# Kernel tuning notes

Measured on AMD Instinct MI355X. Metric: run time of the kernel, lower is better.

## Reference

```python
import jax, jax.numpy as jnp
import numpy as np
import math

B, N, C, H, CH = 1, 256, 128, 4, 32  # batch, n_res, pair channels, heads, head dim
LN_EPS = 1e-5


def setup_inputs() -> dict:
    key = jax.random.key(0)
    ks = jax.random.split(key, 12)
    s = 0.02
    return {
        "act": jax.random.normal(ks[0], (B, N, N, C), dtype=jnp.float32),
        "mask": (jax.random.uniform(ks[1], (B, N, N)) < 0.9).astype(jnp.float32),
        "ln_g": jnp.ones((C,), jnp.float32),
        "ln_b": jnp.zeros((C,), jnp.float32),
        "wq": jax.random.normal(ks[2], (C, H * CH), jnp.float32) * s,
        "wk": jax.random.normal(ks[3], (C, H * CH), jnp.float32) * s,
        "wv": jax.random.normal(ks[4], (C, H * CH), jnp.float32) * s,
        "w2d": jax.random.normal(ks[5], (C, H), jnp.float32) * s,
        "wg": jax.random.normal(ks[6], (C, H * CH), jnp.float32) * s,
        "bg": jnp.ones((H * CH,), jnp.float32),
        "wo": jax.random.normal(ks[7], (H * CH, C), jnp.float32) * s,
        "bo": jnp.zeros((C,), jnp.float32),
    }


def reference(act, mask, ln_g, ln_b, wq, wk, wv, w2d, wg, bg, wo, bo):
    # swap the two residue axes: attend along the *starting* node axis
    x = jnp.swapaxes(act, -2, -3)          # [b, m, i, C]
    m = jnp.swapaxes(mask, -1, -2)         # [b, m, i]
    # LayerNorm
    mu = jnp.mean(x, axis=-1, keepdims=True)
    var = jnp.var(x, axis=-1, keepdims=True)
    x = (x - mu) * jax.lax.rsqrt(var + LN_EPS) * ln_g + ln_b
    # additive mask bias: [b, m, 1, 1, i]
    bias = (1e9 * (m - 1.0))[..., :, None, None, :]
    shp = x.shape[:-1]
    q = (x @ wq).reshape(*shp, H, CH)
    k = (x @ wk).reshape(*shp, H, CH)
    v = (x @ wv).reshape(*shp, H, CH)
    factor = 1.0 / math.sqrt(CH)
    aff = jnp.einsum('bmihc,bmjhc->bmhij', q * factor, k) + bias
    # non-batched pair bias: [b, h, m, i]; broadcasts against [b, m, h, i, j]
    # exactly as in the torch code (requires b == 1)
    nb = jnp.transpose(x @ w2d, (0, 3, 1, 2))
    weights = jax.nn.softmax(aff + nb, axis=-1)  # [b, m, h, i, j]
    g = jax.nn.sigmoid((x @ wg + bg).reshape(*shp, H, CH))
    out = jnp.einsum('bmhqk,bmkhc->bmqhc', weights, v) * g
    out = out.reshape(*shp, H * CH) @ wo + bo
    return jnp.swapaxes(out, -2, -3)
```

## Files before the change

kernel.cpp:

```cpp
#include <hip/hip_runtime.h>
#include <hip/hip_bf16.h>
#include <math.h>


typedef __attribute__((ext_vector_type(8))) short short8;
typedef __attribute__((ext_vector_type(4))) short short4v;
typedef __attribute__((ext_vector_type(4))) float f32x4;

__device__ __forceinline__ unsigned short f2bf(float f) {
  __hip_bfloat16 b = __float2bfloat16(f);
  return __builtin_bit_cast(unsigned short, b);
}
__device__ __forceinline__ float bf2f(unsigned short u) {
  return __uint_as_float(((unsigned int)u) << 16);
}

__device__ __forceinline__ f32x4 mfma16(short8 a, short8 b, f32x4 c) {
  return __builtin_amdgcn_mfma_f32_16x16x32_bf16(a, b, c, 0, 0, 0);
}

__global__ __launch_bounds__(256) void k_conv(const float* __restrict__ wq,
                                              const float* __restrict__ wk,
                                              const float* __restrict__ wv,
                                              const float* __restrict__ wg,
                                              const float* __restrict__ w2d,
                                              const float* __restrict__ wo,
                                              const float* __restrict__ mask,
                                              unsigned short* __restrict__ Wt4,
                                              unsigned short* __restrict__ Wto,
                                              float* __restrict__ maskT) {
  int idx = blockIdx.x * 256 + threadIdx.x;
  if (idx < 65536) {
    int n = idx >> 7, k = idx & 127;
    const float* ws = (n < 128) ? wq : (n < 256) ? wk : (n < 384) ? wv : wg;
    Wt4[idx] = f2bf(ws[k * 128 + (n & 127)]);
  } else if (idx < 73728) {
    int j = idx - 65536;
    int r = j >> 7, k = j & 127;
    Wt4[idx] = (r < 4) ? f2bf(w2d[k * 4 + r]) : (unsigned short)0;
  } else if (idx < 90112) {
    int j = idx - 73728;
    int n = j >> 7, k = j & 127;
    Wto[j] = f2bf(wo[k * 128 + n]);
  } else if (idx < 155648) {
    int j2 = idx - 90112;
    int mi = j2 & 255, jj = j2 >> 8;
    maskT[mi * 256 + jj] = 1e9f * (mask[jj * 256 + mi] - 1.0f);
  }
}

__global__ __launch_bounds__(256) void k_ln(const float* __restrict__ act,
                                            const float* __restrict__ ln_g,
                                            const float* __restrict__ ln_b,
                                            unsigned short* __restrict__ lnxb) {
  int t = threadIdx.x;
  int grp = t >> 4, l16 = t & 15;
  int row = blockIdx.x * 16 + grp;
  int mm = row >> 8, ii = row & 255;
  const float4* a = (const float4*)(act + ((size_t)(ii * 256 + mm)) * 128);
  float4 v0 = a[l16 * 2], v1 = a[l16 * 2 + 1];
  float s = (v0.x + v0.y) + (v0.z + v0.w) + (v1.x + v1.y) + (v1.z + v1.w);
  #pragma unroll
  for (int off = 1; off < 16; off <<= 1) s += __shfl_xor(s, off, 64);
  float mean = s * (1.f / 128.f);
  float e[8] = {v0.x - mean, v0.y - mean, v0.z - mean, v0.w - mean,
                v1.x - mean, v1.y - mean, v1.z - mean, v1.w - mean};
  float vs = (e[0]*e[0] + e[1]*e[1]) + (e[2]*e[2] + e[3]*e[3]) +
             (e[4]*e[4] + e[5]*e[5]) + (e[6]*e[6] + e[7]*e[7]);
  #pragma unroll
  for (int off = 1; off < 16; off <<= 1) vs += __shfl_xor(vs, off, 64);
  float rstd = rsqrtf(vs * (1.f / 128.f) + 1e-5f);
  const float4* gp = (const float4*)ln_g;
  const float4* bp = (const float4*)ln_b;
  float4 g0 = gp[l16 * 2], g1 = gp[l16 * 2 + 1];
  float4 b0 = bp[l16 * 2], b1 = bp[l16 * 2 + 1];
  short8 o;
  o[0] = (short)f2bf(e[0] * rstd * g0.x + b0.x);
  o[1] = (short)f2bf(e[1] * rstd * g0.y + b0.y);
  o[2] = (short)f2bf(e[2] * rstd * g0.z + b0.z);
  o[3] = (short)f2bf(e[3] * rstd * g0.w + b0.w);
  o[4] = (short)f2bf(e[4] * rstd * g1.x + b1.x);
  o[5] = (short)f2bf(e[5] * rstd * g1.y + b1.y);
  o[6] = (short)f2bf(e[6] * rstd * g1.z + b1.z);
  o[7] = (short)f2bf(e[7] * rstd * g1.w + b1.w);
  *(short8*)(lnxb + (size_t)row * 128 + l16 * 8) = o;
}

__global__ __launch_bounds__(256) void k_projg(const unsigned short* __restrict__ A,
                                               const unsigned short* __restrict__ Bt,
                                               const float* __restrict__ bg,
                                               unsigned short* __restrict__ qb,
                                               unsigned short* __restrict__ kb,
                                               unsigned short* __restrict__ vb,
                                               unsigned short* __restrict__ sgb,
                                               float* __restrict__ b2t) {
  __shared__ unsigned short As[128 * 40];
  __shared__ unsigned short Bs[64 * 40];
  int t = threadIdx.x;
  int m0 = blockIdx.x * 128, n0 = blockIdx.y * 64;
  int w = t >> 6, l = t & 63, g = l >> 4, li = l & 15;
  int wr = w >> 1, wc = w & 1;
  f32x4 acc[4][2] = {};
  for (int s = 0; s < 4; ++s) {
    int k0 = s * 32;
    __syncthreads();
    {
      int row = t >> 1, kl = (t & 1) * 16;
      const short8* src = (const short8*)(A + (size_t)(m0 + row) * 128 + k0 + kl);
      *(short8*)&As[row * 40 + kl]     = src[0];
      *(short8*)&As[row * 40 + kl + 8] = src[1];
      int bn = t >> 2, bk = (t & 3) * 8;
      *(short8*)&Bs[bn * 40 + bk] = *(const short8*)(Bt + (size_t)(n0 + bn) * 128 + k0 + bk);
    }
    __syncthreads();
    short8 af[4], bf[2];
    #pragma unroll
    for (int it = 0; it < 4; ++it)
      af[it] = *(const short8*)&As[(wr * 64 + it * 16 + li) * 40 + g * 8];
    #pragma unroll
    for (int jt = 0; jt < 2; ++jt)
      bf[jt] = *(const short8*)&Bs[(wc * 32 + jt * 16 + li) * 40 + g * 8];
    #pragma unroll
    for (int it = 0; it < 4; ++it)
      #pragma unroll
      for (int jt = 0; jt < 2; ++jt)
        acc[it][jt] = mfma16(af[it], bf[jt], acc[it][jt]);
  }
  int which = n0 >> 7;
  if (which == 4) {
    #pragma unroll
    for (int it = 0; it < 4; ++it)
      #pragma unroll
      for (int jt = 0; jt < 2; ++jt) {
        int hb = (wc * 32 + jt * 16 + li);
        if (hb < 4) {
          #pragma unroll
          for (int r = 0; r < 4; ++r) {
            int R = m0 + wr * 64 + it * 16 + g * 4 + r;
            b2t[(size_t)hb * 65536 + (R & 255) * 256 + (R >> 8)] = acc[it][jt][r];
          }
        }
      }
    return;
  }
  const float factor = 0.17677669529663687f;
  #pragma unroll
  for (int it = 0; it < 4; ++it)
    #pragma unroll
    for (int jt = 0; jt < 2; ++jt) {
      int n = n0 + wc * 32 + jt * 16 + li;
      int hh = (n >> 5) & 3, ch = n & 31;
      #pragma unroll
      for (int r = 0; r < 4; ++r) {
        int R = m0 + wr * 64 + it * 16 + g * 4 + r;
        int mm = R >> 8, ii = R & 255;
        size_t o = ((size_t)((mm * 4 + hh) * 256 + ii)) * 32 + ch;
        float v = acc[it][jt][r];
        if (which == 0)      qb[o] = f2bf(v * factor);
        else if (which == 1) kb[o] = f2bf(v);
        else if (which == 2) vb[o] = f2bf(v);
        else                 sgb[o] = f2bf(1.f / (1.f + __expf(-(v + bg[n & 127]))));
      }
    }
}

__global__ __launch_bounds__(256) void k_attn(const unsigned short* __restrict__ qb,
                                              const unsigned short* __restrict__ kb,
                                              const unsigned short* __restrict__ vb,
                                              const unsigned short* __restrict__ sgb,
                                              const float* __restrict__ b2t,
                                              const float* __restrict__ maskT,
                                              unsigned short* __restrict__ aob) {
  __shared__ unsigned short VT[32 * 264];
  __shared__ unsigned short Pl[4 * 32 * 72];
  __shared__ float maskls[256];
  int m = blockIdx.x >> 1, ihalf = blockIdx.x & 1, h = blockIdx.y;
  int t = threadIdx.x, w = t >> 6, l = t & 63, g = l >> 4, li = l & 15;
  int base = (m * 4 + h) << 8;
  maskls[t] = maskT[m * 256 + t];
  {
    const unsigned int* v32 = (const unsigned int*)(vb + (size_t)base * 32);
    #pragma unroll
    for (int p = 0; p < 16; ++p) {
      int idx = t + p * 256;
      int j = idx >> 4, cp = idx & 15;
      unsigned int u = v32[idx];
      VT[(cp * 2) * 264 + j]     = (unsigned short)(u & 0xffff);
      VT[(cp * 2 + 1) * 264 + j] = (unsigned short)(u >> 16);
    }
  }
  __syncthreads();
  int i0 = ihalf * 128 + w * 32;
  short8 qf[2];
  #pragma unroll
  for (int it = 0; it < 2; ++it)
    qf[it] = *(const short8*)(qb + ((size_t)(base + i0 + it * 16 + li)) * 32 + g * 8);
  float mst[2] = {-1e30f, -1e30f};
  float lst[2] = {0.f, 0.f};
  f32x4 oacc[2][2] = {};
  const float* b2 = b2t + (size_t)h * 65536;
  unsigned short* Pw = Pl + w * 32 * 72;
  for (int jc = 0; jc < 4; ++jc) {
    int j0 = jc * 64;
    f32x4 sacc[4][2];
    #pragma unroll
    for (int jt = 0; jt < 4; ++jt) {
      short8 kf = *(const short8*)(kb + ((size_t)(base + j0 + jt * 16 + li)) * 32 + g * 8);
      #pragma unroll
      for (int it = 0; it < 2; ++it) {
        f32x4 z = {0.f, 0.f, 0.f, 0.f};
        sacc[jt][it] = mfma16(kf, qf[it], z);
      }
    }
    #pragma unroll
    for (int it = 0; it < 2; ++it) {
      int ic = i0 + it * 16 + li;
      float s[16];
      float cmax = -1e30f;
      #pragma unroll
      for (int jt = 0; jt < 4; ++jt) {
        int jb = j0 + jt * 16 + g * 4;
        f32x4 mk = *(const f32x4*)&maskls[jb];
        #pragma unroll
        for (int r = 0; r < 4; ++r) {
          float sv = sacc[jt][it][r] + b2[(size_t)(jb + r) * 256 + ic] + mk[r];
          s[jt * 4 + r] = sv;
          cmax = fmaxf(cmax, sv);
        }
      }
      cmax = fmaxf(cmax, __shfl_xor(cmax, 16));
      cmax = fmaxf(cmax, __shfl_xor(cmax, 32));
      float mnew = fmaxf(mst[it], cmax);
      float fac = __expf(mst[it] - mnew);
      mst[it] = mnew;
      lst[it] *= fac;
      oacc[0][it] *= fac;
      oacc[1][it] *= fac;
      float psum = 0.f;
      #pragma unroll
      for (int jt = 0; jt < 4; ++jt) {
        float p0 = __expf(s[jt * 4 + 0] - mnew);
        float p1 = __expf(s[jt * 4 + 1] - mnew);
        float p2 = __expf(s[jt * 4 + 2] - mnew);
        float p3 = __expf(s[jt * 4 + 3] - mnew);
        psum += p0 + p1 + p2 + p3;
        short4v pk;
        pk.x = (short)f2bf(p0); pk.y = (short)f2bf(p1);
        pk.z = (short)f2bf(p2); pk.w = (short)f2bf(p3);
        *(short4v*)&Pw[(it * 16 + li) * 72 + jt * 16 + g * 4] = pk;
      }
      lst[it] += psum;
    }
    asm volatile("" ::: "memory");
    #pragma unroll
    for (int ks = 0; ks < 2; ++ks) {
      short8 vf0 = *(const short8*)&VT[li * 264        + j0 + ks * 32 + g * 8];
      short8 vf1 = *(const short8*)&VT[(16 + li) * 264 + j0 + ks * 32 + g * 8];
      #pragma unroll
      for (int it = 0; it < 2; ++it) {
        short8 pf = *(const short8*)&Pw[(it * 16 + li) * 72 + ks * 32 + g * 8];
        oacc[0][it] = mfma16(vf0, pf, oacc[0][it]);
        oacc[1][it] = mfma16(vf1, pf, oacc[1][it]);
      }
    }
    asm volatile("" ::: "memory");
  }
  #pragma unroll
  for (int it = 0; it < 2; ++it) {
    float lt = lst[it];
    lt += __shfl_xor(lt, 16);
    lt += __shfl_xor(lt, 32);
    float inv = 1.f / lt;
    int ic = i0 + it * 16 + li;
    #pragma unroll
    for (int ct = 0; ct < 2; ++ct) {
      int c0 = ct * 16 + g * 4;
      const unsigned short* grow = sgb + ((size_t)(base + ic)) * 32 + c0;
      ushort4 gu = *(const ushort4*)grow;
      ushort4 ov;
      ov.x = f2bf(oacc[ct][it][0] * inv * bf2f(gu.x));
      ov.y = f2bf(oacc[ct][it][1] * inv * bf2f(gu.y));
      ov.z = f2bf(oacc[ct][it][2] * inv * bf2f(gu.z));
      ov.w = f2bf(oacc[ct][it][3] * inv * bf2f(gu.w));
      *(ushort4*)&aob[((size_t)(ic * 256 + m)) * 128 + h * 32 + c0] = ov;
    }
  }
}

__global__ __launch_bounds__(256) void k_outg(const unsigned short* __restrict__ A,
                                              const unsigned short* __restrict__ Bt,
                                              const float* __restrict__ bo,
                                              float* __restrict__ out) {
  __shared__ unsigned short As[128 * 40];
  __shared__ unsigned short Bs[64 * 40];
  int t = threadIdx.x;
  int m0 = blockIdx.x * 128, n0 = blockIdx.y * 64;
  int w = t >> 6, l = t & 63, g = l >> 4, li = l & 15;
  int wr = w >> 1, wc = w & 1;
  f32x4 acc[4][2] = {};
  for (int s = 0; s < 4; ++s) {
    int k0 = s * 32;
    __syncthreads();
    {
      int row = t >> 1, kl = (t & 1) * 16;
      const short8* src = (const short8*)(A + (size_t)(m0 + row) * 128 + k0 + kl);
      *(short8*)&As[row * 40 + kl]     = src[0];
      *(short8*)&As[row * 40 + kl + 8] = src[1];
      int bn = t >> 2, bk = (t & 3) * 8;
      *(short8*)&Bs[bn * 40 + bk] = *(const short8*)(Bt + (size_t)(n0 + bn) * 128 + k0 + bk);
    }
    __syncthreads();
    short8 af[4], bf[2];
    #pragma unroll
    for (int it = 0; it < 4; ++it)
      af[it] = *(const short8*)&As[(wr * 64 + it * 16 + li) * 40 + g * 8];
    #pragma unroll
    for (int jt = 0; jt < 2; ++jt)
      bf[jt] = *(const short8*)&Bs[(wc * 32 + jt * 16 + li) * 40 + g * 8];
    #pragma unroll
    for (int it = 0; it < 4; ++it)
      #pragma unroll
      for (int jt = 0; jt < 2; ++jt)
        acc[it][jt] = mfma16(af[it], bf[jt], acc[it][jt]);
  }
  #pragma unroll
  for (int it = 0; it < 4; ++it)
    #pragma unroll
    for (int jt = 0; jt < 2; ++jt) {
      int n = n0 + wc * 32 + jt * 16 + li;
      float bias = bo[n];
      #pragma unroll
      for (int r = 0; r < 4; ++r) {
        int R = m0 + wr * 64 + it * 16 + g * 4 + r;
        out[(size_t)R * 128 + n] = acc[it][jt][r] + bias;
      }
    }
}

extern "C" void kernel_launch(void* const* d_in, const int* in_sizes, int n_in,
                              void* d_out, int out_size, void* d_ws, size_t ws_size,
                              hipStream_t stream) {
  const float* act  = (const float*)d_in[0];
  const float* mask = (const float*)d_in[1];
  const float* ln_g = (const float*)d_in[2];
  const float* ln_b = (const float*)d_in[3];
  const float* wq   = (const float*)d_in[4];
  const float* wk   = (const float*)d_in[5];
  const float* wv   = (const float*)d_in[6];
  const float* w2d  = (const float*)d_in[7];
  const float* wg   = (const float*)d_in[8];
  const float* bg   = (const float*)d_in[9];
  const float* wo   = (const float*)d_in[10];
  const float* bo   = (const float*)d_in[11];

  char* p = (char*)d_ws;
  unsigned short* lnxb  = (unsigned short*)p;  p += (size_t)8388608 * 2;
  float*          b2t   = (float*)p;           p += (size_t)262144 * 4;
  unsigned short* qb    = (unsigned short*)p;  p += (size_t)8388608 * 2;
  unsigned short* kb    = (unsigned short*)p;  p += (size_t)8388608 * 2;
  unsigned short* vb    = (unsigned short*)p;  p += (size_t)8388608 * 2;
  unsigned short* sgb   = (unsigned short*)p;  p += (size_t)8388608 * 2;
  unsigned short* aob   = (unsigned short*)p;  p += (size_t)8388608 * 2;
  unsigned short* Wt4   = (unsigned short*)p;  p += (size_t)73728 * 2;
  unsigned short* Wto   = (unsigned short*)p;  p += (size_t)16384 * 2;
  float*          maskT = (float*)p;           p += (size_t)65536 * 4;
  float* out = (float*)d_out;

  hipLaunchKernelGGL(k_conv,  dim3(608),      dim3(256), 0, stream, wq, wk, wv, wg, w2d, wo, mask, Wt4, Wto, maskT);
  hipLaunchKernelGGL(k_ln,    dim3(4096),     dim3(256), 0, stream, act, ln_g, ln_b, lnxb);
  hipLaunchKernelGGL(k_projg, dim3(512, 9),   dim3(256), 0, stream, lnxb, Wt4, bg, qb, kb, vb, sgb, b2t);
  hipLaunchKernelGGL(k_attn,  dim3(512, 4),   dim3(256), 0, stream, qb, kb, vb, sgb, b2t, maskT, aob);
  hipLaunchKernelGGL(k_outg,  dim3(512, 2),   dim3(256), 0, stream, aob, Wto, bo, out);
}
```

Measured before the change: 104.0 us.

## Merge weight conversion into LayerNorm launch and vectorize GEMM epilogue stores

Folds the weight/mask conversion kernel into the LayerNorm kernel as extra blocks, which removes one launch. It also swaps the MFMA operand order so each lane holds four consecutive output columns. The projection and output epilogues can then write packed 4-wide bf16 or float4 stores instead of scalar strided stores. The pair-bias path is rewritten to match the transposed accumulator layout.

```diff
diff --git a/kernel.cpp b/kernel.cpp
--- a/kernel.cpp
+++ b/kernel.cpp
@@ -19,41 +19,42 @@
   return __builtin_amdgcn_mfma_f32_16x16x32_bf16(a, b, c, 0, 0, 0);
 }
 
-__global__ __launch_bounds__(256) void k_conv(const float* __restrict__ wq,
-                                              const float* __restrict__ wk,
-                                              const float* __restrict__ wv,
-                                              const float* __restrict__ wg,
-                                              const float* __restrict__ w2d,
-                                              const float* __restrict__ wo,
-                                              const float* __restrict__ mask,
-                                              unsigned short* __restrict__ Wt4,
-                                              unsigned short* __restrict__ Wto,
-                                              float* __restrict__ maskT) {
-  int idx = blockIdx.x * 256 + threadIdx.x;
-  if (idx < 65536) {
-    int n = idx >> 7, k = idx & 127;
-    const float* ws = (n < 128) ? wq : (n < 256) ? wk : (n < 384) ? wv : wg;
-    Wt4[idx] = f2bf(ws[k * 128 + (n & 127)]);
-  } else if (idx < 73728) {
-    int j = idx - 65536;
-    int r = j >> 7, k = j & 127;
-    Wt4[idx] = (r < 4) ? f2bf(w2d[k * 4 + r]) : (unsigned short)0;
-  } else if (idx < 90112) {
-    int j = idx - 73728;
-    int n = j >> 7, k = j & 127;
-    Wto[j] = f2bf(wo[k * 128 + n]);
-  } else if (idx < 155648) {
-    int j2 = idx - 90112;
-    int mi = j2 & 255, jj = j2 >> 8;
-    maskT[mi * 256 + jj] = 1e9f * (mask[jj * 256 + mi] - 1.0f);
-  }
-}
-
 __global__ __launch_bounds__(256) void k_ln(const float* __restrict__ act,
                                             const float* __restrict__ ln_g,
                                             const float* __restrict__ ln_b,
-                                            unsigned short* __restrict__ lnxb) {
+                                            const float* __restrict__ wq,
+                                            const float* __restrict__ wk,
+                                            const float* __restrict__ wv,
+                                            const float* __restrict__ wg,
+                                            const float* __restrict__ w2d,
+                                            const float* __restrict__ wo,
+                                            const float* __restrict__ mask,
+                                            unsigned short* __restrict__ lnxb,
+                                            unsigned short* __restrict__ Wt4,
+                                            unsigned short* __restrict__ Wto,
+                                            float* __restrict__ maskT) {
   int t = threadIdx.x;
+  if (blockIdx.x >= 4096) {
+    int idx = (blockIdx.x - 4096) * 256 + t;
+    if (idx < 65536) {
+      int n = idx >> 7, k = idx & 127;
+      const float* ws = (n < 128) ? wq : (n < 256) ? wk : (n < 384) ? wv : wg;
+      Wt4[idx] = f2bf(ws[k * 128 + (n & 127)]);
+    } else if (idx < 73728) {
+      int j = idx - 65536;
+      int r = j >> 7, k = j & 127;
+      Wt4[idx] = (r < 4) ? f2bf(w2d[k * 4 + r]) : (unsigned short)0;
+    } else if (idx < 90112) {
+      int j = idx - 73728;
+      int n = j >> 7, k = j & 127;
+      Wto[j] = f2bf(wo[k * 128 + n]);
+    } else if (idx < 155648) {
+      int j2 = idx - 90112;
+      int mi = j2 & 255, jj = j2 >> 8;
+      maskT[mi * 256 + jj] = 1e9f * (mask[jj * 256 + mi] - 1.0f);
+    }
+    return;
+  }
   int grp = t >> 4, l16 = t & 15;
   int row = blockIdx.x * 16 + grp;
   int mm = row >> 8, ii = row & 255;
@@ -124,44 +125,53 @@
     for (int it = 0; it < 4; ++it)
       #pragma unroll
       for (int jt = 0; jt < 2; ++jt)
-        acc[it][jt] = mfma16(af[it], bf[jt], acc[it][jt]);
+        acc[it][jt] = mfma16(bf[jt], af[it], acc[it][jt]);
   }
   int which = n0 >> 7;
   if (which == 4) {
-    #pragma unroll
-    for (int it = 0; it < 4; ++it)
-      #pragma unroll
-      for (int jt = 0; jt < 2; ++jt) {
-        int hb = (wc * 32 + jt * 16 + li);
-        if (hb < 4) {
-          #pragma unroll
-          for (int r = 0; r < 4; ++r) {
-            int R = m0 + wr * 64 + it * 16 + g * 4 + r;
-            b2t[(size_t)hb * 65536 + (R & 255) * 256 + (R >> 8)] = acc[it][jt][r];
-          }
-        }
-      }
+    if (wc == 0 && g == 0) {
+      #pragma unroll
+      for (int it = 0; it < 4; ++it) {
+        int R = m0 + wr * 64 + it * 16 + li;
+        int mm = R >> 8, ii = R & 255;
+        #pragma unroll
+        for (int r = 0; r < 4; ++r)
+          b2t[(size_t)r * 65536 + ii * 256 + mm] = acc[it][0][r];
+      }
+    }
     return;
   }
   const float factor = 0.17677669529663687f;
   #pragma unroll
-  for (int it = 0; it < 4; ++it)
+  for (int it = 0; it < 4; ++it) {
+    int R = m0 + wr * 64 + it * 16 + li;
+    int mm = R >> 8, ii = R & 255;
     #pragma unroll
     for (int jt = 0; jt < 2; ++jt) {
-      int n = n0 + wc * 32 + jt * 16 + li;
-      int hh = (n >> 5) & 3, ch = n & 31;
-      #pragma unroll
-      for (int r = 0; r < 4; ++r) {
-        int R = m0 + wr * 64 + it * 16 + g * 4 + r;
-        int mm = R >> 8, ii = R & 255;
-        size_t o = ((size_t)((mm * 4 + hh) * 256 + ii)) * 32 + ch;
-        float v = acc[it][jt][r];
-        if (which == 0)      qb[o] = f2bf(v * factor);
-        else if (which == 1) kb[o] = f2bf(v);
-        else if (which == 2) vb[o] = f2bf(v);
-        else                 sgb[o] = f2bf(1.f / (1.f + __expf(-(v + bg[n & 127]))));
-      }
-    }
+      int nb4 = n0 + wc * 32 + jt * 16 + g * 4;
+      int hh = (nb4 >> 5) & 3, ch = nb4 & 31;
+      size_t o = ((size_t)((mm * 4 + hh) * 256 + ii)) * 32 + ch;
+      short4v pk;
+      if (which == 0) {
+        #pragma unroll
+        for (int r = 0; r < 4; ++r) pk[r] = (short)f2bf(acc[it][jt][r] * factor);
+        *(short4v*)(qb + o) = pk;
+      } else if (which == 1) {
+        #pragma unroll
+        for (int r = 0; r < 4; ++r) pk[r] = (short)f2bf(acc[it][jt][r]);
+        *(short4v*)(kb + o) = pk;
+      } else if (which == 2) {
+        #pragma unroll
+        for (int r = 0; r < 4; ++r) pk[r] = (short)f2bf(acc[it][jt][r]);
+        *(short4v*)(vb + o) = pk;
+      } else {
+        #pragma unroll
+        for (int r = 0; r < 4; ++r)
+          pk[r] = (short)f2bf(1.f / (1.f + __expf(-(acc[it][jt][r] + bg[(nb4 & 127) + r]))));
+        *(short4v*)(sgb + o) = pk;
+      }
+    }
+  }
 }
 
 __global__ __launch_bounds__(256) void k_attn(const unsigned short* __restrict__ qb,
@@ -321,20 +331,22 @@
     for (int it = 0; it < 4; ++it)
       #pragma unroll
       for (int jt = 0; jt < 2; ++jt)
-        acc[it][jt] = mfma16(af[it], bf[jt], acc[it][jt]);
-  }
-  #pragma unroll
-  for (int it = 0; it < 4; ++it)
+        acc[it][jt] = mfma16(bf[jt], af[it], acc[it][jt]);
+  }
+  #pragma unroll
+  for (int it = 0; it < 4; ++it) {
+    int R = m0 + wr * 64 + it * 16 + li;
     #pragma unroll
     for (int jt = 0; jt < 2; ++jt) {
-      int n = n0 + wc * 32 + jt * 16 + li;
-      float bias = bo[n];
-      #pragma unroll
-      for (int r = 0; r < 4; ++r) {
-        int R = m0 + wr * 64 + it * 16 + g * 4 + r;
-        out[(size_t)R * 128 + n] = acc[it][jt][r] + bias;
-      }
-    }
+      int nb4 = n0 + wc * 32 + jt * 16 + g * 4;
+      float4 o;
+      o.x = acc[it][jt][0] + bo[nb4 + 0];
+      o.y = acc[it][jt][1] + bo[nb4 + 1];
+      o.z = acc[it][jt][2] + bo[nb4 + 2];
+      o.w = acc[it][jt][3] + bo[nb4 + 3];
+      *(float4*)(out + (size_t)R * 128 + nb4) = o;
+    }
+  }
 }
 
 extern "C" void kernel_launch(void* const* d_in, const int* in_sizes, int n_in,
@@ -366,8 +378,8 @@
   float*          maskT = (float*)p;           p += (size_t)65536 * 4;
   float* out = (float*)d_out;
 
-  hipLaunchKernelGGL(k_conv,  dim3(608),      dim3(256), 0, stream, wq, wk, wv, wg, w2d, wo, mask, Wt4, Wto, maskT);
-  hipLaunchKernelGGL(k_ln,    dim3(4096),     dim3(256), 0, stream, act, ln_g, ln_b, lnxb);
+  hipLaunchKernelGGL(k_ln,    dim3(4704),     dim3(256), 0, stream,
+                     act, ln_g, ln_b, wq, wk, wv, wg, w2d, wo, mask, lnxb, Wt4, Wto, maskT);
   hipLaunchKernelGGL(k_projg, dim3(512, 9),   dim3(256), 0, stream, lnxb, Wt4, bg, qb, kb, vb, sgb, b2t);
   hipLaunchKernelGGL(k_attn,  dim3(512, 4),   dim3(256), 0, stream, qb, kb, vb, sgb, b2t, maskT, aob);
   hipLaunchKernelGGL(k_outg,  dim3(512, 2),   dim3(256), 0, stream, aob, Wto, bo, out);
```

Measured after the change: 95.72 us. -8.0%, faster.
